# Kernel tuning notes

Measured on AMD Instinct MI355X. Metric: run time of the kernel, lower is better.

The kernel has to match this reference:

```python
import jax, jax.numpy as jnp
import numpy as np

T = 500_000  # sequence length
K = 16       # number of hidden states


def setup_inputs() -> dict:
    key = jax.random.key(0)
    k1, k2, k3, k4 = jax.random.split(key, 4)
    y = jax.random.normal(k1, (T,), dtype=jnp.float32)
    transition_logits = jax.random.normal(k2, (K, K), dtype=jnp.float32)
    mu = 2.0 * jax.random.normal(k3, (K,), dtype=jnp.float32)
    log_sigma = 0.1 * jax.random.normal(k4, (K,), dtype=jnp.float32)
    return {"y": y, "transition_logits": transition_logits, "mu": mu, "log_sigma": log_sigma}


def _stationary_distribution(P):
    # Solve pi P = pi, sum(pi) = 1 via least squares (normal equations: differentiable, jit-safe).
    k = P.shape[0]
    A = jnp.concatenate([P.T - jnp.eye(k, dtype=P.dtype), jnp.ones((1, k), dtype=P.dtype)], axis=0)
    b = jnp.concatenate([jnp.zeros((k,), dtype=P.dtype), jnp.ones((1,), dtype=P.dtype)])
    return jnp.linalg.solve(A.T @ A, A.T @ b)


def reference(y, transition_logits, mu, log_sigma):
    P = jax.nn.softmax(transition_logits, axis=-1)  # [K, K] row-stochastic transition matrix
    sigma = jnp.exp(log_sigma)
    # Gaussian emission densities g[t, k] = N(y_t; mu_k, sigma_k^2)
    z = (y[:, None] - mu[None, :]) / sigma[None, :]
    INV_SQRT_2PI = 0.3989422804014327
    g = jnp.exp(-0.5 * z * z) * (INV_SQRT_2PI / sigma)[None, :]  # [T, K]

    ut0 = _stationary_distribution(P)              # [K]
    g0 = g[0]
    ft0 = jnp.sum(ut0 * g0)                        # scalar
    utt0 = ut0 * g0 / ft0                          # [K]

    def step(utt_prev, gt):
        ut = utt_prev @ P                          # predictive dist [K]
        ft = jnp.sum(ut * gt)                      # normalizer
        utt = ut * gt / ft                         # filtered posterior [K]
        return utt, (ut, ft, utt)

    _, (Ut, ft_rest, Utt) = jax.lax.scan(step, utt0, g[1:])

    ut = jnp.concatenate([ut0[None, :], Ut], axis=0)       # [T, K]
    u_norm = jnp.concatenate([utt0[None, :], Utt], axis=0)  # [T, K]
    ft = jnp.concatenate([ft0[None], ft_rest], axis=0)      # [T]
    return (ut, u_norm, ft)
```

## Files before the change

### kernel.cpp

```cpp
#include <hip/hip_runtime.h>

#define CHUNK_L 32
#define WARMUP_W 16

typedef float v2f __attribute__((ext_vector_type(2)));

template<int K> __device__ __forceinline__ float bcast16(float v) {
    return __int_as_float(__builtin_amdgcn_update_dpp(
        0, __float_as_int(v), 0x150 | K, 0xF, 0xF, true));
}
template<int N> __device__ __forceinline__ float rowror16(float v) {
    return __int_as_float(__builtin_amdgcn_update_dpp(
        0, __float_as_int(v), 0x120 | N, 0xF, 0xF, true));
}

__device__ __forceinline__ float rowsum16(float p) {
    p += rowror16<1>(p);
    p += rowror16<2>(p);
    p += rowror16<4>(p);
    p += rowror16<8>(p);
    return p;
}

__device__ __forceinline__ float dot16(float a, const v2f* pc2) {
    v2f b0, b1, u01, u23;
    b0.x = bcast16<0>(a);  b0.y = bcast16<1>(a);
    b1.x = bcast16<2>(a);  b1.y = bcast16<3>(a);
    u01 = b0 * pc2[0];
    u23 = b1 * pc2[1];
    b0.x = bcast16<4>(a);  b0.y = bcast16<5>(a);
    b1.x = bcast16<6>(a);  b1.y = bcast16<7>(a);
    u01 = b0 * pc2[2] + u01;
    u23 = b1 * pc2[3] + u23;
    b0.x = bcast16<8>(a);  b0.y = bcast16<9>(a);
    b1.x = bcast16<10>(a); b1.y = bcast16<11>(a);
    u01 = b0 * pc2[4] + u01;
    u23 = b1 * pc2[5] + u23;
    b0.x = bcast16<12>(a); b0.y = bcast16<13>(a);
    b1.x = bcast16<14>(a); b1.y = bcast16<15>(a);
    u01 = b0 * pc2[6] + u01;
    u23 = b1 * pc2[7] + u23;
    v2f u = u01 + u23;
    return u.x + u.y;
}

__global__ __launch_bounds__(256, 4) void hmm_filter_kernel(
    const float* __restrict__ y,
    const float* __restrict__ logits,
    const float* __restrict__ mu,
    const float* __restrict__ log_sigma,
    float* __restrict__ out,
    int T, int nchunks)
{
    __shared__ float Plds[256];
    __shared__ float Ba[256];
    __shared__ float Bb[256];

    const int tid = (int)threadIdx.x;
    const int j   = tid & 15;
    const int g   = tid >> 4;

    float l = logits[tid];
    float m = l;
    #pragma unroll
    for (int s = 1; s < 16; s <<= 1) m = fmaxf(m, __shfl_xor(m, s, 16));
    float e = __expf(l - m);
    float rs = e;
    #pragma unroll
    for (int s = 1; s < 16; s <<= 1) rs += __shfl_xor(rs, s, 16);
    float Pv = e / rs;
    Plds[tid] = Pv;
    Ba[tid]   = Pv;
    __syncthreads();

    float* cur = Ba;
    float* nxt = Bb;
    for (int itq = 0; itq < 10; ++itq) {
        float acc = 0.f;
        #pragma unroll
        for (int k = 0; k < 16; ++k)
            acc += cur[g * 16 + k] * cur[k * 16 + j];
        float rsum = acc;
        #pragma unroll
        for (int s = 1; s < 16; s <<= 1) rsum += __shfl_xor(rsum, s, 16);
        nxt[tid] = acc / rsum;
        __syncthreads();
        float* tmp = cur; cur = nxt; nxt = tmp;
    }

    const float api = cur[j];

    v2f pc2[8];
    #pragma unroll
    for (int k = 0; k < 8; ++k) {
        pc2[k].x = Plds[(2 * k)     * 16 + j];
        pc2[k].y = Plds[(2 * k + 1) * 16 + j];
    }

    const float muj = mu[j];
    const float isj = __expf(-log_sigma[j]);
    const float nmj = -muj * isj;
    const float lcf = __log2f(0.3989422804014327f * isj);
    const float K2  = -0.7213475204444817f;

    const int chunk = (int)blockIdx.x * 16 + g;
    if (chunk >= nchunks) return;

    const int wfrom = chunk * CHUNK_L;
    int t0 = wfrom - WARMUP_W; if (t0 < 0) t0 = 0;
    const int nwb = (wfrom - t0) >> 2;
    const int Tm4 = T - 4;
    const int TN  = T << 4;

    auto emis = [&](float yt) -> float {
        float z = fmaf(yt, isj, nmj);
        return __builtin_amdgcn_exp2f(fmaf(z * z, K2, lcf));
    };

    float p = api;
    int t = t0;

    float4 c4 = *(const float4*)(y + t);
    int pf = t + 4; if (pf > Tm4) pf = Tm4;
    float4 n1 = *(const float4*)(y + pf);

    for (int b = 0; b < nwb; ++b) {
        int p2 = t + 8; if (p2 > Tm4) p2 = Tm4;
        const float4 n2 = *(const float4*)(y + p2);
        p = dot16(p, pc2) * emis(c4.x);
        p = dot16(p, pc2) * emis(c4.y);
        p = dot16(p, pc2) * emis(c4.z);
        p = dot16(p, pc2) * emis(c4.w);
        if (b == 1) p *= __builtin_amdgcn_rcpf(rowsum16(p));
        c4 = n1; n1 = n2; t += 4;
    }
    p *= __builtin_amdgcn_rcpf(rowsum16(p));

    float* __restrict__ pU = out + (wfrom << 4) + j;
    float* __restrict__ pN = pU + TN;
    float* __restrict__ pF = out + 2 * TN + wfrom;

    #pragma unroll 1
    for (int b = 0; b < (CHUNK_L / 4); ++b) {
        int p2 = t + 8; if (p2 > Tm4) p2 = Tm4;
        const float4 n2 = *(const float4*)(y + p2);

        const float q0  = dot16(p, pc2);
        const float pg0 = q0 * emis(c4.x);
        const float s0  = rowsum16(pg0);
        const float r0  = __builtin_amdgcn_rcpf(s0);
        const float q1  = dot16(pg0, pc2);
        const float pg1 = q1 * emis(c4.y);
        const float s1  = rowsum16(pg1);
        const float r1  = __builtin_amdgcn_rcpf(s1);
        const float q2  = dot16(pg1, pc2);
        const float pg2 = q2 * emis(c4.z);
        const float s2  = rowsum16(pg2);
        const float r2  = __builtin_amdgcn_rcpf(s2);
        const float q3  = dot16(pg2, pc2);
        const float pg3 = q3 * emis(c4.w);
        const float s3  = rowsum16(pg3);
        const float r3  = __builtin_amdgcn_rcpf(s3);

        pU[0]  = q0;
        pU[16] = q1 * r0;
        pU[32] = q2 * r1;
        pU[48] = q3 * r2;
        pN[0]  = pg0 * r0;
        pN[16] = pg1 * r1;
        pN[32] = pg2 * r2;
        const float utt3 = pg3 * r3;
        pN[48] = utt3;
        if (j == 0)
            *(float4*)pF = make_float4(s0, s1 * r0, s2 * r1, s3 * r2);

        p = utt3;
        pU += 64; pN += 64; pF += 4;
        c4 = n1; n1 = n2; t += 4;
    }
}

extern "C" void kernel_launch(void* const* d_in, const int* in_sizes, int n_in,
                              void* d_out, int out_size, void* d_ws, size_t ws_size,
                              hipStream_t stream) {
    const float* y      = (const float*)d_in[0];
    const float* logits = (const float*)d_in[1];
    const float* mu     = (const float*)d_in[2];
    const float* ls     = (const float*)d_in[3];
    float* out = (float*)d_out;
    const int T = in_sizes[0];

    const int nchunks = (T + CHUNK_L - 1) / CHUNK_L;
    const int blocks  = (nchunks + 15) / 16;
    hmm_filter_kernel<<<blocks, 256, 0, stream>>>(y, logits, mu, ls, out,
                                                  T, nchunks);
}
```

Baseline: 95.24 us.

## Take per-step normalization off the recurrence chain and prefetch y earlier

The serial filter chain no longer waits on the row-sum reduction and reciprocal at each step. The unnormalized posterior is propagated, and the scale correction is folded into the next block's first emission and into the stored outputs, so the rowsum/rcp work can overlap the next dot products. It also issues the first y loads before the P-power iteration to hide their latency, and deepens the y prefetch to four float4 loads ahead. The cost is more live registers and more intricate scale bookkeeping, where unnormalized magnitudes could drift within a block.

```diff
diff --git a/kernel.cpp b/kernel.cpp
--- a/kernel.cpp
+++ b/kernel.cpp
@@ -71,6 +71,20 @@
     float Pv = e / rs;
     Plds[tid] = Pv;
     Ba[tid]   = Pv;
+
+    const int chunk = (int)blockIdx.x * 16 + g;
+    const int wfrom = chunk * CHUNK_L;
+    int t0 = wfrom - WARMUP_W; if (t0 < 0) t0 = 0;
+    const int Tm4 = T - 4;
+    int ta = t0; if (ta > Tm4) ta = Tm4;
+    int a1 = ta + 4;  if (a1 > Tm4) a1 = Tm4;
+    int a2 = ta + 8;  if (a2 > Tm4) a2 = Tm4;
+    int a3 = ta + 12; if (a3 > Tm4) a3 = Tm4;
+    float4 c4 = *(const float4*)(y + ta);
+    float4 n1 = *(const float4*)(y + a1);
+    float4 n2 = *(const float4*)(y + a2);
+    float4 n3 = *(const float4*)(y + a3);
+
     __syncthreads();
 
     float* cur = Ba;
@@ -103,13 +117,9 @@
     const float lcf = __log2f(0.3989422804014327f * isj);
     const float K2  = -0.7213475204444817f;
 
-    const int chunk = (int)blockIdx.x * 16 + g;
     if (chunk >= nchunks) return;
 
-    const int wfrom = chunk * CHUNK_L;
-    int t0 = wfrom - WARMUP_W; if (t0 < 0) t0 = 0;
     const int nwb = (wfrom - t0) >> 2;
-    const int Tm4 = T - 4;
     const int TN  = T << 4;
 
     auto emis = [&](float yt) -> float {
@@ -120,63 +130,72 @@
     float p = api;
     int t = t0;
 
-    float4 c4 = *(const float4*)(y + t);
-    int pf = t + 4; if (pf > Tm4) pf = Tm4;
-    float4 n1 = *(const float4*)(y + pf);
-
+    float rw = 1.f;
     for (int b = 0; b < nwb; ++b) {
-        int p2 = t + 8; if (p2 > Tm4) p2 = Tm4;
-        const float4 n2 = *(const float4*)(y + p2);
-        p = dot16(p, pc2) * emis(c4.x);
+        int p4 = t + 16; if (p4 > Tm4) p4 = Tm4;
+        const float4 nn = *(const float4*)(y + p4);
+        float e0w = emis(c4.x);
+        if (b == 2) e0w *= rw;
+        p = dot16(p, pc2) * e0w;
         p = dot16(p, pc2) * emis(c4.y);
         p = dot16(p, pc2) * emis(c4.z);
         p = dot16(p, pc2) * emis(c4.w);
-        if (b == 1) p *= __builtin_amdgcn_rcpf(rowsum16(p));
-        c4 = n1; n1 = n2; t += 4;
-    }
-    p *= __builtin_amdgcn_rcpf(rowsum16(p));
+        if (b == 1) rw = __builtin_amdgcn_rcpf(rowsum16(p));
+        c4 = n1; n1 = n2; n2 = n3; n3 = nn; t += 4;
+    }
+    const float rcm = __builtin_amdgcn_rcpf(rowsum16(p));
 
     float* __restrict__ pU = out + (wfrom << 4) + j;
     float* __restrict__ pN = pU + TN;
     float* __restrict__ pF = out + 2 * TN + wfrom;
 
+    float r1p = rcm;
+    float r3p = rcm;
+    float w   = 1.f;
+
     #pragma unroll 1
     for (int b = 0; b < (CHUNK_L / 4); ++b) {
-        int p2 = t + 8; if (p2 > Tm4) p2 = Tm4;
-        const float4 n2 = *(const float4*)(y + p2);
+        int p4 = t + 16; if (p4 > Tm4) p4 = Tm4;
+        const float4 nn = *(const float4*)(y + p4);
+
+        const float e0 = emis(c4.x) * r1p;
 
         const float q0  = dot16(p, pc2);
-        const float pg0 = q0 * emis(c4.x);
-        const float s0  = rowsum16(pg0);
-        const float r0  = __builtin_amdgcn_rcpf(s0);
+        const float pg0 = q0 * e0;
         const float q1  = dot16(pg0, pc2);
         const float pg1 = q1 * emis(c4.y);
-        const float s1  = rowsum16(pg1);
-        const float r1  = __builtin_amdgcn_rcpf(s1);
         const float q2  = dot16(pg1, pc2);
         const float pg2 = q2 * emis(c4.z);
-        const float s2  = rowsum16(pg2);
-        const float r2  = __builtin_amdgcn_rcpf(s2);
         const float q3  = dot16(pg2, pc2);
         const float pg3 = q3 * emis(c4.w);
-        const float s3  = rowsum16(pg3);
-        const float r3  = __builtin_amdgcn_rcpf(s3);
-
-        pU[0]  = q0;
+
+        const float s0 = rowsum16(pg0);
+        const float r0 = __builtin_amdgcn_rcpf(s0);
+        const float s1 = rowsum16(pg1);
+        const float r1 = __builtin_amdgcn_rcpf(s1);
+        const float s2 = rowsum16(pg2);
+        const float r2 = __builtin_amdgcn_rcpf(s2);
+        const float s3 = rowsum16(pg3);
+        const float r3 = __builtin_amdgcn_rcpf(s3);
+
+        pU[0]  = q0 * r3p;
         pU[16] = q1 * r0;
         pU[32] = q2 * r1;
         pU[48] = q3 * r2;
         pN[0]  = pg0 * r0;
         pN[16] = pg1 * r1;
         pN[32] = pg2 * r2;
-        const float utt3 = pg3 * r3;
-        pN[48] = utt3;
+        pN[48] = pg3 * r3;
         if (j == 0)
-            *(float4*)pF = make_float4(s0, s1 * r0, s2 * r1, s3 * r2);
-
-        p = utt3;
+            *(float4*)pF = make_float4(s0 * w, s1 * r0, s2 * r1, s3 * r2);
+
+        p   = pg3;
+        w   = s1 * r3;
+        r1p = r1;
+        r3p = r3;
+
         pU += 64; pN += 64; pF += 4;
-        c4 = n1; n1 = n2; t += 4;
+        c4 = n1; n1 = n2; n2 = n3; n3 = nn; t += 4;
     }
 }
 
```

After: 95.58 us. About the same (+0.4%).

## Batch chunk recurrences through MFMA with split-fp16 transition matrix

Applied to the files above, without the earlier changes.

Replaces the per-chunk DPP broadcast dot products with a 16x16x16 fp16 MFMA, where each wave processes 16 chunks as the 16 columns of the matrix. It keeps near-fp32 accuracy by splitting P and the state into hi/lo fp16 parts and issuing three MFMAs per step. Normalisation is deferred by one step, and chunk 0's warmup is handled by forcing its emissions to 1. This trades the VALU and cross-lane broadcast cost for matrix-core latency and some rounding error. It also changes the store pattern so each lane writes four states for one chunk.

```diff
diff --git a/kernel.cpp b/kernel.cpp
--- a/kernel.cpp
+++ b/kernel.cpp
@@ -3,45 +3,19 @@
 #define CHUNK_L 32
 #define WARMUP_W 16
 
-typedef float v2f __attribute__((ext_vector_type(2)));
-
-template<int K> __device__ __forceinline__ float bcast16(float v) {
-    return __int_as_float(__builtin_amdgcn_update_dpp(
-        0, __float_as_int(v), 0x150 | K, 0xF, 0xF, true));
-}
-template<int N> __device__ __forceinline__ float rowror16(float v) {
-    return __int_as_float(__builtin_amdgcn_update_dpp(
-        0, __float_as_int(v), 0x120 | N, 0xF, 0xF, true));
-}
-
-__device__ __forceinline__ float rowsum16(float p) {
-    p += rowror16<1>(p);
-    p += rowror16<2>(p);
-    p += rowror16<4>(p);
-    p += rowror16<8>(p);
-    return p;
-}
-
-__device__ __forceinline__ float dot16(float a, const v2f* pc2) {
-    v2f b0, b1, u01, u23;
-    b0.x = bcast16<0>(a);  b0.y = bcast16<1>(a);
-    b1.x = bcast16<2>(a);  b1.y = bcast16<3>(a);
-    u01 = b0 * pc2[0];
-    u23 = b1 * pc2[1];
-    b0.x = bcast16<4>(a);  b0.y = bcast16<5>(a);
-    b1.x = bcast16<6>(a);  b1.y = bcast16<7>(a);
-    u01 = b0 * pc2[2] + u01;
-    u23 = b1 * pc2[3] + u23;
-    b0.x = bcast16<8>(a);  b0.y = bcast16<9>(a);
-    b1.x = bcast16<10>(a); b1.y = bcast16<11>(a);
-    u01 = b0 * pc2[4] + u01;
-    u23 = b1 * pc2[5] + u23;
-    b0.x = bcast16<12>(a); b0.y = bcast16<13>(a);
-    b1.x = bcast16<14>(a); b1.y = bcast16<15>(a);
-    u01 = b0 * pc2[6] + u01;
-    u23 = b1 * pc2[7] + u23;
-    v2f u = u01 + u23;
-    return u.x + u.y;
+typedef _Float16 h16;
+typedef _Float16 h16x4 __attribute__((ext_vector_type(4)));
+typedef float f32x4 __attribute__((ext_vector_type(4)));
+
+static __device__ __forceinline__ f32x4 mfma16(h16x4 a, h16x4 b, f32x4 c) {
+#if __has_builtin(__builtin_amdgcn_mfma_f32_16x16x16f16)
+    return __builtin_amdgcn_mfma_f32_16x16x16f16(a, b, c, 0, 0, 0);
+#else
+    f32x4 d;
+    asm volatile("v_mfma_f32_16x16x16_f16 %0, %1, %2, %3\n\ts_nop 7\n\ts_nop 7"
+                 : "=v"(d) : "v"(a), "v"(b), "v"(c));
+    return d;
+#endif
 }
 
 __global__ __launch_bounds__(256, 4) void hmm_filter_kernel(
@@ -58,7 +32,7 @@
 
     const int tid = (int)threadIdx.x;
     const int j   = tid & 15;
-    const int g   = tid >> 4;
+    const int gr  = tid >> 4;
 
     float l = logits[tid];
     float m = l;
@@ -79,7 +53,7 @@
         float acc = 0.f;
         #pragma unroll
         for (int k = 0; k < 16; ++k)
-            acc += cur[g * 16 + k] * cur[k * 16 + j];
+            acc += cur[gr * 16 + k] * cur[k * 16 + j];
         float rsum = acc;
         #pragma unroll
         for (int s = 1; s < 16; s <<= 1) rsum += __shfl_xor(rsum, s, 16);
@@ -88,96 +62,124 @@
         float* tmp = cur; cur = nxt; nxt = tmp;
     }
 
-    const float api = cur[j];
-
-    v2f pc2[8];
-    #pragma unroll
-    for (int k = 0; k < 8; ++k) {
-        pc2[k].x = Plds[(2 * k)     * 16 + j];
-        pc2[k].y = Plds[(2 * k + 1) * 16 + j];
-    }
-
-    const float muj = mu[j];
-    const float isj = __expf(-log_sigma[j]);
-    const float nmj = -muj * isj;
-    const float lcf = __log2f(0.3989422804014327f * isj);
-    const float K2  = -0.7213475204444817f;
-
-    const int chunk = (int)blockIdx.x * 16 + g;
-    if (chunk >= nchunks) return;
-
-    const int wfrom = chunk * CHUNK_L;
-    int t0 = wfrom - WARMUP_W; if (t0 < 0) t0 = 0;
-    const int nwb = (wfrom - t0) >> 2;
+    const int lane = tid & 63;
+    const int col  = lane & 15;
+    const int i0   = (lane >> 4) << 2;
+    const int wv   = ((int)blockIdx.x << 2) + (tid >> 6);
+    const int cbase = wv << 4;
+
+    h16x4 Ahi, Alo;
+    #pragma unroll
+    for (int ee = 0; ee < 4; ++ee) {
+        float a = Plds[(i0 + ee) * 16 + col];
+        h16 hi = (h16)a;
+        Ahi[ee] = hi;
+        Alo[ee] = (h16)(a - (float)hi);
+    }
+
+    h16x4 bhi, blo;
+    #pragma unroll
+    for (int ee = 0; ee < 4; ++ee) {
+        float pv = cur[i0 + ee];
+        h16 hi = (h16)pv;
+        bhi[ee] = hi;
+        blo[ee] = (h16)(pv - (float)hi);
+    }
+
+    float isv[4], nmv[4], lcv[4];
+    #pragma unroll
+    for (int ee = 0; ee < 4; ++ee) {
+        int st = i0 + ee;
+        float is = __expf(-log_sigma[st]);
+        isv[ee] = is;
+        nmv[ee] = -mu[st] * is;
+        lcv[ee] = __log2f(0.3989422804014327f * is);
+    }
+    const float K2 = -0.7213475204444817f;
+
+    if (cbase >= nchunks) return;
+
+    const int chunk = cbase + col;
+    const bool live = chunk < nchunks;
+    const bool isC0 = (chunk == 0);
     const int Tm4 = T - 4;
     const int TN  = T << 4;
 
-    auto emis = [&](float yt) -> float {
-        float z = fmaf(yt, isj, nmj);
-        return __builtin_amdgcn_exp2f(fmaf(z * z, K2, lcf));
+    int tb = chunk * CHUNK_L - WARMUP_W;
+
+    auto yld = [&](int t) -> float4 {
+        int tc = t < 0 ? 0 : (t > Tm4 ? Tm4 : t);
+        return *(const float4*)(y + tc);
     };
 
-    float p = api;
-    int t = t0;
-
-    float4 c4 = *(const float4*)(y + t);
-    int pf = t + 4; if (pf > Tm4) pf = Tm4;
-    float4 n1 = *(const float4*)(y + pf);
-
-    for (int b = 0; b < nwb; ++b) {
-        int p2 = t + 8; if (p2 > Tm4) p2 = Tm4;
-        const float4 n2 = *(const float4*)(y + p2);
-        p = dot16(p, pc2) * emis(c4.x);
-        p = dot16(p, pc2) * emis(c4.y);
-        p = dot16(p, pc2) * emis(c4.z);
-        p = dot16(p, pc2) * emis(c4.w);
-        if (b == 1) p *= __builtin_amdgcn_rcpf(rowsum16(p));
-        c4 = n1; n1 = n2; t += 4;
-    }
-    p *= __builtin_amdgcn_rcpf(rowsum16(p));
-
-    float* __restrict__ pU = out + (wfrom << 4) + j;
-    float* __restrict__ pN = pU + TN;
-    float* __restrict__ pF = out + 2 * TN + wfrom;
-
+    float4 c4 = yld(tb);
+    float4 n1 = yld(tb + 4);
+
+    float r1 = 1.0f;
+
+#define FSTEP(YT, WARM, DOST, UTP, UNP, FDST)  do {                       \
+    f32x4 D = {0.f, 0.f, 0.f, 0.f};                                       \
+    D = mfma16(Ahi, bhi, D);                                              \
+    D = mfma16(Alo, bhi, D);                                              \
+    D = mfma16(Ahi, blo, D);                                              \
+    f32x4 eg;                                                             \
+    _Pragma("unroll")                                                     \
+    for (int ee = 0; ee < 4; ++ee) {                                      \
+        float z  = fmaf((YT), isv[ee], nmv[ee]);                          \
+        float gg = __builtin_amdgcn_exp2f(fmaf(z * z, K2, lcv[ee]));      \
+        if (WARM) gg = isC0 ? 1.0f : gg;                                  \
+        eg[ee] = gg * r1;                                                 \
+    }                                                                     \
+    f32x4 pg = D * eg;                                                    \
+    float sv = (pg.x + pg.y) + (pg.z + pg.w);                             \
+    sv += __shfl_xor(sv, 16);                                             \
+    sv += __shfl_xor(sv, 32);                                             \
+    float rv = __builtin_amdgcn_rcpf(sv);                                 \
+    if ((DOST) && live) {                                                 \
+        f32x4 ut = D * r1;                                                \
+        f32x4 un = pg * rv;                                               \
+        *(f32x4*)(UTP) = ut;                                              \
+        *(f32x4*)(UNP) = un;                                              \
+    }                                                                     \
+    if (DOST) { FDST = sv; }                                              \
+    _Pragma("unroll")                                                     \
+    for (int ee = 0; ee < 4; ++ee) {                                      \
+        h16 hh = (h16)pg[ee];                                             \
+        bhi[ee] = hh;                                                     \
+        blo[ee] = (h16)(pg[ee] - (float)hh);                              \
+    }                                                                     \
+    r1 = rv;                                                              \
+} while (0)
+
+    float fdummy;
     #pragma unroll 1
-    for (int b = 0; b < (CHUNK_L / 4); ++b) {
-        int p2 = t + 8; if (p2 > Tm4) p2 = Tm4;
-        const float4 n2 = *(const float4*)(y + p2);
-
-        const float q0  = dot16(p, pc2);
-        const float pg0 = q0 * emis(c4.x);
-        const float s0  = rowsum16(pg0);
-        const float r0  = __builtin_amdgcn_rcpf(s0);
-        const float q1  = dot16(pg0, pc2);
-        const float pg1 = q1 * emis(c4.y);
-        const float s1  = rowsum16(pg1);
-        const float r1  = __builtin_amdgcn_rcpf(s1);
-        const float q2  = dot16(pg1, pc2);
-        const float pg2 = q2 * emis(c4.z);
-        const float s2  = rowsum16(pg2);
-        const float r2  = __builtin_amdgcn_rcpf(s2);
-        const float q3  = dot16(pg2, pc2);
-        const float pg3 = q3 * emis(c4.w);
-        const float s3  = rowsum16(pg3);
-        const float r3  = __builtin_amdgcn_rcpf(s3);
-
-        pU[0]  = q0;
-        pU[16] = q1 * r0;
-        pU[32] = q2 * r1;
-        pU[48] = q3 * r2;
-        pN[0]  = pg0 * r0;
-        pN[16] = pg1 * r1;
-        pN[32] = pg2 * r2;
-        const float utt3 = pg3 * r3;
-        pN[48] = utt3;
-        if (j == 0)
-            *(float4*)pF = make_float4(s0, s1 * r0, s2 * r1, s3 * r2);
-
-        p = utt3;
+    for (int b = 0; b < WARMUP_W / 4; ++b) {
+        float4 nn = yld(tb + 8);
+        FSTEP(c4.x, true, false, out, out, fdummy);
+        FSTEP(c4.y, true, false, out, out, fdummy);
+        FSTEP(c4.z, true, false, out, out, fdummy);
+        FSTEP(c4.w, true, false, out, out, fdummy);
+        c4 = n1; n1 = nn; tb += 4;
+    }
+    (void)fdummy;
+
+    float* pU = out + ((chunk * CHUNK_L) << 4) + i0;
+    float* pN = pU + TN;
+    float* pF = out + 2 * TN + chunk * CHUNK_L;
+    f32x4 f4;
+
+    #pragma unroll 1
+    for (int b = 0; b < CHUNK_L / 4; ++b) {
+        float4 nn = yld(tb + 8);
+        FSTEP(c4.x, false, true, pU,      pN,      f4.x);
+        FSTEP(c4.y, false, true, pU + 16, pN + 16, f4.y);
+        FSTEP(c4.z, false, true, pU + 32, pN + 32, f4.z);
+        FSTEP(c4.w, false, true, pU + 48, pN + 48, f4.w);
+        if (lane < 16 && live) *(f32x4*)(pF) = f4;
         pU += 64; pN += 64; pF += 4;
-        c4 = n1; n1 = n2; t += 4;
-    }
+        c4 = n1; n1 = nn; tb += 4;
+    }
+#undef FSTEP
 }
 
 extern "C" void kernel_launch(void* const* d_in, const int* in_sizes, int n_in,
@@ -191,7 +193,8 @@
     const int T = in_sizes[0];
 
     const int nchunks = (T + CHUNK_L - 1) / CHUNK_L;
-    const int blocks  = (nchunks + 15) / 16;
+    const int nwaves  = (nchunks + 15) / 16;
+    const int blocks  = (nwaves + 3) / 4;
     hmm_filter_kernel<<<blocks, 256, 0, stream>>>(y, logits, mu, ls, out,
                                                   T, nchunks);
 }
```

Result: faster. 89.64 us (-5.9%).
